# Optimization experiments

Measured on AMD Instinct MI355X. Metric: run time of the kernel, lower is better.

## Reference

```python
import jax, jax.numpy as jnp
import numpy as np

N_HEAD = 16

def setup_inputs() -> dict:
    key = jax.random.key(0)
    ks = jax.random.split(key, 5)
    C = 1024
    x = jax.random.normal(ks[0], (2, 2048, C), dtype=jnp.float32)
    w_attn = jax.random.normal(ks[1], (C, 3 * C), dtype=jnp.float32) * (C ** -0.5)
    b_attn = jax.random.normal(ks[2], (3 * C,), dtype=jnp.float32) * 0.02
    w_proj = jax.random.normal(ks[3], (C, C), dtype=jnp.float32) * (C ** -0.5)
    b_proj = jax.random.normal(ks[4], (C,), dtype=jnp.float32) * 0.02
    return {"x": x, "w_attn": w_attn, "b_attn": b_attn, "w_proj": w_proj, "b_proj": b_proj}

def reference(x, w_attn, b_attn, w_proj, b_proj):
    B, T, C = x.shape
    H = N_HEAD
    D = C // H  # head_dim
    qkv = x @ w_attn + b_attn  # [B,T,3C]
    q, k, v = jnp.split(qkv, 3, axis=-1)
    # [B,T,H,D] -> [B,H,T,D]
    q = q.reshape(B, T, H, D).transpose(0, 2, 1, 3)
    k = k.reshape(B, T, H, D).transpose(0, 2, 1, 3)
    v = v.reshape(B, T, H, D).transpose(0, 2, 1, 3)
    scale = 1.0 / np.sqrt(D).astype(np.float32)
    att = jnp.einsum('bhqd,bhkd->bhqk', q, k) * scale  # [B,H,T,T]
    causal = jnp.tril(jnp.ones((T, T), dtype=bool))
    att = jnp.where(causal, att, jnp.finfo(att.dtype).min)
    att = jax.nn.softmax(att, axis=-1)
    y = jnp.einsum('bhqk,bhkd->bhqd', att, v)  # [B,H,T,D]
    y = y.transpose(0, 2, 1, 3).reshape(B, T, C)
    return y @ w_proj + b_proj
```

## Files before the change

kernel.cpp:

```cpp
#include <hip/hip_runtime.h>
#include <hip/hip_bf16.h>
#include <stdint.h>

typedef __bf16 bf16x8 __attribute__((ext_vector_type(8)));
typedef __bf16 bf16x4 __attribute__((ext_vector_type(4)));
typedef float  f32x4  __attribute__((ext_vector_type(4)));

#define GLOBAL_AS __attribute__((address_space(1)))
#define LDS_AS    __attribute__((address_space(3)))

__device__ __forceinline__ void gld_lds16(const __bf16* g, __bf16* l) {
  __builtin_amdgcn_global_load_lds((GLOBAL_AS void*)g, (LDS_AS void*)l, 16, 0, 0);
}

#define QSCALE 0.18033688011116029f

__device__ __forceinline__ unsigned pk2(float a, float b) {
  unsigned short ua = __builtin_bit_cast(unsigned short, (__bf16)a);
  unsigned short ub = __builtin_bit_cast(unsigned short, (__bf16)b);
  return (unsigned)ua | ((unsigned)ub << 16);
}

union PackU { unsigned u[4]; bf16x8 v; };

__global__ __launch_bounds__(256) void cast_bf16_kernel(const float* __restrict__ src,
                                                        __bf16* __restrict__ dst, int n)
{
  int i = (blockIdx.x * 256 + threadIdx.x) * 8;
  if (i >= n) return;
  float4 a = *(const float4*)(src + i);
  float4 b = *(const float4*)(src + i + 4);
  bf16x8 o;
  o[0]=(__bf16)a.x; o[1]=(__bf16)a.y; o[2]=(__bf16)a.z; o[3]=(__bf16)a.w;
  o[4]=(__bf16)b.x; o[5]=(__bf16)b.y; o[6]=(__bf16)b.z; o[7]=(__bf16)b.w;
  *(bf16x8*)(dst + i) = o;
}

__global__ __launch_bounds__(256) void transpose_cast_kernel(const float* __restrict__ src,
                                                             __bf16* __restrict__ dst,
                                                             int R, int C)
{
  __shared__ float tile[32][33];
  int c0 = blockIdx.x * 32, r0 = blockIdx.y * 32;
  int tx = threadIdx.x & 31, ty = threadIdx.x >> 5;
  #pragma unroll
  for (int i = 0; i < 32; i += 8)
    tile[ty + i][tx] = src[(size_t)(r0 + ty + i) * C + (c0 + tx)];
  __syncthreads();
  #pragma unroll
  for (int i = 0; i < 32; i += 8)
    dst[(size_t)(c0 + ty + i) * R + (r0 + tx)] = (__bf16)tile[tx][ty + i];
}

template<int MODE, int BM>
__global__ __launch_bounds__(256, (BM == 128 ? 3 : 2))
void gemm_kernel(const __bf16* __restrict__ A,
                 const __bf16* __restrict__ Bt,
                 const float*  __restrict__ bias,
                 float* __restrict__ outF,
                 __bf16* __restrict__ qb,
                 __bf16* __restrict__ kb,
                 __bf16* __restrict__ vb,
                 int M, int N, int K)
{
  __shared__ __bf16 As[BM * 64];
  __shared__ __bf16 Bs[128 * 64];
  const int tid  = threadIdx.x;
  const int wave = tid >> 6, lane = tid & 63;
  const int lo = lane & 15, g4 = lane >> 4;
  const int bm = blockIdx.y * BM;
  const int bn = blockIdx.x * 128;
  const int wr = (wave >> 1) * (BM / 2);
  const int wc = (wave & 1) * 64;
  constexpr int MF = BM / 32;

  f32x4 acc[MF][4] = {};

  const int nkt = K >> 6;
  for (int kt = 0; kt < nkt; ++kt) {
    const int k0 = kt << 6;
    __syncthreads();
    #pragma unroll
    for (int j = 0; j < BM / 32; ++j) {
      int c = j * 256 + tid;
      int r = c >> 3, cc = c & 7;
      int cs = cc ^ (r & 7);
      gld_lds16(A + (size_t)(bm + r) * K + (k0 + cs * 8), As + c * 8);
    }
    #pragma unroll
    for (int j = 0; j < 4; ++j) {
      int c = j * 256 + tid;
      int r = c >> 3, cc = c & 7;
      int cs = cc ^ (r & 7);
      gld_lds16(Bt + (size_t)(bn + r) * K + (k0 + cs * 8), Bs + c * 8);
    }
    __syncthreads();
    #pragma unroll
    for (int ks = 0; ks < 2; ++ks) {
      bf16x8 af[MF], bfr[4];
      #pragma unroll
      for (int mf = 0; mf < MF; ++mf) {
        int row = wr + mf * 16 + lo;
        int ch = (ks * 4 + g4) ^ (row & 7);
        af[mf] = *(const bf16x8*)(As + row * 64 + ch * 8);
      }
      #pragma unroll
      for (int nf = 0; nf < 4; ++nf) {
        int row = wc + nf * 16 + lo;
        int ch = (ks * 4 + g4) ^ (row & 7);
        bfr[nf] = *(const bf16x8*)(Bs + row * 64 + ch * 8);
      }
      #pragma unroll
      for (int mf = 0; mf < MF; ++mf)
        #pragma unroll
        for (int nf = 0; nf < 4; ++nf)
          acc[mf][nf] = __builtin_amdgcn_mfma_f32_16x16x32_bf16(af[mf], bfr[nf], acc[mf][nf], 0, 0, 0);
    }
  }

  float bv[4];
  #pragma unroll
  for (int nf = 0; nf < 4; ++nf) bv[nf] = bias[bn + wc + nf * 16 + lo];

  if (MODE == 1) {
    #pragma unroll
    for (int mf = 0; mf < MF; ++mf)
      #pragma unroll
      for (int nf = 0; nf < 4; ++nf) {
        int col = bn + wc + nf * 16 + lo;
        #pragma unroll
        for (int j = 0; j < 4; ++j) {
          int row = bm + wr + mf * 16 + g4 * 4 + j;
          outF[(size_t)row * N + col] = acc[mf][nf][j] + bv[nf];
        }
      }
  } else {
    #pragma unroll
    for (int mf = 0; mf < MF; ++mf) {
      const int tbase = bm + wr + mf * 16 + g4 * 4;
      const int b = tbase >> 11, t = tbase & 2047;
      #pragma unroll
      for (int nf = 0; nf < 4; ++nf) {
        int n = bn + wc + nf * 16 + lo;
        int sel = n >> 10, hd = n & 1023;
        int h = hd >> 6, d = hd & 63;
        size_t bh = (size_t)(b * 16 + h);
        if (sel == 2) {
          bf16x4 pv;
          #pragma unroll
          for (int j = 0; j < 4; ++j) pv[j] = (__bf16)(acc[mf][nf][j] + bv[nf]);
          *(bf16x4*)(vb + (bh * 64 + d) * 2048 + t) = pv;
        } else if (sel == 0) {
          #pragma unroll
          for (int j = 0; j < 4; ++j)
            qb[(bh * 2048 + (size_t)(t + j)) * 64 + d] = (__bf16)((acc[mf][nf][j] + bv[nf]) * QSCALE);
        } else {
          #pragma unroll
          for (int j = 0; j < 4; ++j)
            kb[(bh * 2048 + (size_t)(t + j)) * 64 + d] = (__bf16)(acc[mf][nf][j] + bv[nf]);
        }
      }
    }
  }
}

__global__ __launch_bounds__(256, 4)
void attn_kernel(const __bf16* __restrict__ qg, const __bf16* __restrict__ kg,
                 const __bf16* __restrict__ vg, __bf16* __restrict__ yg)
{
  const int n = blockIdx.x;
  const int xcd = n & 7;
  const int w = n >> 3;
  const int quad = w >> 5;
  const int r = w & 31;
  const int bh = xcd + 8 * (r & 3);
  const int p = r >> 2;
  int strip;
  if      (quad == 0) strip = p;
  else if (quad == 1) strip = 31 - p;
  else if (quad == 2) strip = 8 + p;
  else                strip = 23 - p;
  const int b = bh >> 4, h = bh & 15;

  const int tid  = threadIdx.x;
  const int wave = tid >> 6;
  const int lane = tid & 63;
  const int l15  = lane & 15;
  const int g    = lane >> 4;
  const int sw   = l15 & 7;

  __shared__ __bf16 Kb[2][64 * 64];
  __shared__ __bf16 Vb[2][64 * 64];

  const __bf16* qbase = qg + (size_t)bh * 2048 * 64;
  const __bf16* kbase = kg + (size_t)bh * 2048 * 64;
  const __bf16* vbase = vg + (size_t)bh * 64 * 2048;

  const int q16 = strip * 64 + wave * 16 + l15;
  const bf16x8 qf0 = *(const bf16x8*)(qbase + (size_t)q16 * 64 + g * 8);
  const bf16x8 qf1 = *(const bf16x8*)(qbase + (size_t)q16 * 64 + 32 + g * 8);

  f32x4 o0 = {}, o1 = {}, o2 = {}, o3 = {}, osum = {};

  bf16x8 ones;
  #pragma unroll
  for (int j = 0; j < 8; ++j) ones[j] = (__bf16)1.0f;

  auto STAGE = [&](int kt, int bsel) {
    #pragma unroll
    for (int j = 0; j < 2; ++j) {
      int c = j * 256 + tid;
      int cr = c >> 3, cc = c & 7;
      int cs = cc ^ (cr & 7);
      int pr = (cr & 0x23) | ((cr & 0x10) >> 2) | ((cr & 0x0C) << 1);
      gld_lds16(kbase + (size_t)(kt * 64 + pr) * 64 + cs * 8, &Kb[bsel][0] + c * 8);
      gld_lds16(vbase + (size_t)cr * 2048 + (kt * 64 + cs * 8), &Vb[bsel][0] + c * 8);
    }
  };

  STAGE(0, 0);
  int cur = 0;

  for (int i = 0; i <= strip; ++i) {
    __syncthreads();
    if (i < strip) STAGE(i + 1, cur ^ 1);

    const __bf16* KL = &Kb[cur][0];
    f32x4 s0 = {}, s1 = {}, s2 = {}, s3 = {};
    {
      bf16x8 k00 = *(const bf16x8*)(KL + (0  + l15) * 64 + ((0 + g) ^ sw) * 8);
      bf16x8 k01 = *(const bf16x8*)(KL + (0  + l15) * 64 + ((4 + g) ^ sw) * 8);
      s0 = __builtin_amdgcn_mfma_f32_16x16x32_bf16(k00, qf0, s0, 0, 0, 0);
      s0 = __builtin_amdgcn_mfma_f32_16x16x32_bf16(k01, qf1, s0, 0, 0, 0);
      bf16x8 k10 = *(const bf16x8*)(KL + (16 + l15) * 64 + ((0 + g) ^ sw) * 8);
      bf16x8 k11 = *(const bf16x8*)(KL + (16 + l15) * 64 + ((4 + g) ^ sw) * 8);
      s1 = __builtin_amdgcn_mfma_f32_16x16x32_bf16(k10, qf0, s1, 0, 0, 0);
      s1 = __builtin_amdgcn_mfma_f32_16x16x32_bf16(k11, qf1, s1, 0, 0, 0);
      bf16x8 k20 = *(const bf16x8*)(KL + (32 + l15) * 64 + ((0 + g) ^ sw) * 8);
      bf16x8 k21 = *(const bf16x8*)(KL + (32 + l15) * 64 + ((4 + g) ^ sw) * 8);
      s2 = __builtin_amdgcn_mfma_f32_16x16x32_bf16(k20, qf0, s2, 0, 0, 0);
      s2 = __builtin_amdgcn_mfma_f32_16x16x32_bf16(k21, qf1, s2, 0, 0, 0);
      bf16x8 k30 = *(const bf16x8*)(KL + (48 + l15) * 64 + ((0 + g) ^ sw) * 8);
      bf16x8 k31 = *(const bf16x8*)(KL + (48 + l15) * 64 + ((4 + g) ^ sw) * 8);
      s3 = __builtin_amdgcn_mfma_f32_16x16x32_bf16(k30, qf0, s3, 0, 0, 0);
      s3 = __builtin_amdgcn_mfma_f32_16x16x32_bf16(k31, qf1, s3, 0, 0, 0);
    }

    if (i == strip) {
      const int qr = wave * 16 + l15;
      #pragma unroll
      for (int r2 = 0; r2 < 4; ++r2) {
        if (8 * g + r2          > qr) s0[r2] = -3.0e38f;
        if (8 * g + 4 + r2      > qr) s1[r2] = -3.0e38f;
        if (32 + 8 * g + r2     > qr) s2[r2] = -3.0e38f;
        if (32 + 8 * g + 4 + r2 > qr) s3[r2] = -3.0e38f;
      }
    }

    #pragma unroll
    for (int r2 = 0; r2 < 4; ++r2) s0[r2] = exp2f(s0[r2]);
    #pragma unroll
    for (int r2 = 0; r2 < 4; ++r2) s1[r2] = exp2f(s1[r2]);
    #pragma unroll
    for (int r2 = 0; r2 < 4; ++r2) s2[r2] = exp2f(s2[r2]);
    #pragma unroll
    for (int r2 = 0; r2 < 4; ++r2) s3[r2] = exp2f(s3[r2]);

    PackU pa0, pa1;
    pa0.u[0] = pk2(s0[0], s0[1]); pa0.u[1] = pk2(s0[2], s0[3]);
    pa0.u[2] = pk2(s1[0], s1[1]); pa0.u[3] = pk2(s1[2], s1[3]);
    pa1.u[0] = pk2(s2[0], s2[1]); pa1.u[1] = pk2(s2[2], s2[3]);
    pa1.u[2] = pk2(s3[0], s3[1]); pa1.u[3] = pk2(s3[2], s3[3]);

    osum = __builtin_amdgcn_mfma_f32_16x16x32_bf16(pa0.v, ones, osum, 0, 0, 0);
    osum = __builtin_amdgcn_mfma_f32_16x16x32_bf16(pa1.v, ones, osum, 0, 0, 0);

    const __bf16* VL = &Vb[cur][0];
    {
      bf16x8 v00 = *(const bf16x8*)(VL + (0  + l15) * 64 + ((0 + g) ^ sw) * 8);
      bf16x8 v01 = *(const bf16x8*)(VL + (0  + l15) * 64 + ((4 + g) ^ sw) * 8);
      o0 = __builtin_amdgcn_mfma_f32_16x16x32_bf16(pa0.v, v00, o0, 0, 0, 0);
      o0 = __builtin_amdgcn_mfma_f32_16x16x32_bf16(pa1.v, v01, o0, 0, 0, 0);
      bf16x8 v10 = *(const bf16x8*)(VL + (16 + l15) * 64 + ((0 + g) ^ sw) * 8);
      bf16x8 v11 = *(const bf16x8*)(VL + (16 + l15) * 64 + ((4 + g) ^ sw) * 8);
      o1 = __builtin_amdgcn_mfma_f32_16x16x32_bf16(pa0.v, v10, o1, 0, 0, 0);
      o1 = __builtin_amdgcn_mfma_f32_16x16x32_bf16(pa1.v, v11, o1, 0, 0, 0);
      bf16x8 v20 = *(const bf16x8*)(VL + (32 + l15) * 64 + ((0 + g) ^ sw) * 8);
      bf16x8 v21 = *(const bf16x8*)(VL + (32 + l15) * 64 + ((4 + g) ^ sw) * 8);
      o2 = __builtin_amdgcn_mfma_f32_16x16x32_bf16(pa0.v, v20, o2, 0, 0, 0);
      o2 = __builtin_amdgcn_mfma_f32_16x16x32_bf16(pa1.v, v21, o2, 0, 0, 0);
      bf16x8 v30 = *(const bf16x8*)(VL + (48 + l15) * 64 + ((0 + g) ^ sw) * 8);
      bf16x8 v31 = *(const bf16x8*)(VL + (48 + l15) * 64 + ((4 + g) ^ sw) * 8);
      o3 = __builtin_amdgcn_mfma_f32_16x16x32_bf16(pa0.v, v30, o3, 0, 0, 0);
      o3 = __builtin_amdgcn_mfma_f32_16x16x32_bf16(pa1.v, v31, o3, 0, 0, 0);
    }

    cur ^= 1;
  }

  #pragma unroll
  for (int r2 = 0; r2 < 4; ++r2) {
    float il = 1.0f / osum[r2];
    int trow = strip * 64 + wave * 16 + 4 * g + r2;
    __bf16* dst = yg + ((size_t)(b * 2048 + trow)) * 1024 + h * 64;
    dst[l15]      = (__bf16)(o0[r2] * il);
    dst[16 + l15] = (__bf16)(o1[r2] * il);
    dst[32 + l15] = (__bf16)(o2[r2] * il);
    dst[48 + l15] = (__bf16)(o3[r2] * il);
  }
}

extern "C" void kernel_launch(void* const* d_in, const int* in_sizes, int n_in,
                              void* d_out, int out_size, void* d_ws, size_t ws_size,
                              hipStream_t stream)
{
  const float* x      = (const float*)d_in[0];
  const float* w_attn = (const float*)d_in[1];
  const float* b_attn = (const float*)d_in[2];
  const float* w_proj = (const float*)d_in[3];
  const float* b_proj = (const float*)d_in[4];
  float* out = (float*)d_out;

  __bf16* xb  = (__bf16*)d_ws;
  __bf16* waT = xb  + (size_t)4096 * 1024;
  __bf16* wpT = waT + (size_t)3072 * 1024;
  __bf16* qb  = wpT + (size_t)1024 * 1024;
  __bf16* kb  = qb  + (size_t)32 * 2048 * 64;
  __bf16* vb  = kb  + (size_t)32 * 2048 * 64;
  __bf16* yb  = vb  + (size_t)32 * 2048 * 64;

  cast_bf16_kernel<<<2048, 256, 0, stream>>>(x, xb, 4096 * 1024);
  transpose_cast_kernel<<<dim3(96, 32), 256, 0, stream>>>(w_attn, waT, 1024, 3072);
  transpose_cast_kernel<<<dim3(32, 32), 256, 0, stream>>>(w_proj, wpT, 1024, 1024);
  gemm_kernel<0, 128><<<dim3(24, 32), 256, 0, stream>>>(xb, waT, b_attn, nullptr,
                                                        qb, kb, vb, 4096, 3072, 1024);
  attn_kernel<<<1024, 256, 0, stream>>>(qb, kb, vb, yb);
  gemm_kernel<1, 64><<<dim3(8, 64), 256, 0, stream>>>(yb, wpT, b_proj, out,
                                                      nullptr, nullptr, nullptr, 4096, 1024, 1024);
}
```

Measured before the change: 99.98 us.

## Balance causal attention with split-KV strips and remap QKV GEMM block order

The attention kernel now gives every block a fixed budget of roughly 16-17 key tiles. Blocks with t<16 finish a short strip, then process the first half of a long strip's keys. Blocks with t>=16 process the second half. Partial unnormalized outputs and row sums go to workspace and a new merge kernel combines them. The QKV GEMM also uses a 1D grid with a swizzled block-to-tile mapping to improve L2 locality across XCDs. This adds an extra kernel launch and partial-result traffic, and it reuses the x/weight workspace buffers for partials.

```diff
diff --git a/kernel.cpp b/kernel.cpp
--- a/kernel.cpp
+++ b/kernel.cpp
@@ -68,8 +68,15 @@
   const int tid  = threadIdx.x;
   const int wave = tid >> 6, lane = tid & 63;
   const int lo = lane & 15, g4 = lane >> 4;
-  const int bm = blockIdx.y * BM;
-  const int bn = blockIdx.x * 128;
+  int bm, bn;
+  if (MODE == 0) {
+    int bid = blockIdx.x;
+    int bm_i = (bid & 7) * 4 + ((bid >> 3) & 3);
+    int bn_i = bid >> 5;
+    bm = bm_i * 128; bn = bn_i * 128;
+  } else {
+    bm = blockIdx.y * BM; bn = blockIdx.x * 128;
+  }
   const int wr = (wave >> 1) * (BM / 2);
   const int wc = (wave & 1) * 64;
   constexpr int MF = BM / 32;
@@ -165,21 +172,15 @@
 }
 
 __global__ __launch_bounds__(256, 4)
-void attn_kernel(const __bf16* __restrict__ qg, const __bf16* __restrict__ kg,
-                 const __bf16* __restrict__ vg, __bf16* __restrict__ yg)
+void attn_kernel(const __bf16* __restrict__ qg_, const __bf16* __restrict__ kg,
+                 const __bf16* __restrict__ vg, __bf16* __restrict__ yg,
+                 __bf16* __restrict__ pY, float* __restrict__ pL)
 {
   const int n = blockIdx.x;
   const int xcd = n & 7;
-  const int w = n >> 3;
-  const int quad = w >> 5;
-  const int r = w & 31;
-  const int bh = xcd + 8 * (r & 3);
-  const int p = r >> 2;
-  int strip;
-  if      (quad == 0) strip = p;
-  else if (quad == 1) strip = 31 - p;
-  else if (quad == 2) strip = 8 + p;
-  else                strip = 23 - p;
+  const int m = n >> 3;
+  const int bh = xcd + 8 * (m & 3);
+  const int t = m >> 2;
   const int b = bh >> 4, h = bh & 15;
 
   const int tid  = threadIdx.x;
@@ -192,20 +193,25 @@
   __shared__ __bf16 Kb[2][64 * 64];
   __shared__ __bf16 Vb[2][64 * 64];
 
-  const __bf16* qbase = qg + (size_t)bh * 2048 * 64;
-  const __bf16* kbase = kg + (size_t)bh * 2048 * 64;
-  const __bf16* vbase = vg + (size_t)bh * 64 * 2048;
-
-  const int q16 = strip * 64 + wave * 16 + l15;
-  const bf16x8 qf0 = *(const bf16x8*)(qbase + (size_t)q16 * 64 + g * 8);
-  const bf16x8 qf1 = *(const bf16x8*)(qbase + (size_t)q16 * 64 + 32 + g * 8);
-
-  f32x4 o0 = {}, o1 = {}, o2 = {}, o3 = {}, osum = {};
+  const __bf16* qbase = qg_ + (size_t)bh * 2048 * 64;
+  const __bf16* kbase = kg  + (size_t)bh * 2048 * 64;
+  const __bf16* vbase = vg  + (size_t)bh * 64 * 2048;
+
+  bf16x8 qf0, qf1;
+  f32x4 o0, o1, o2, o3, osum;
 
   bf16x8 ones;
   #pragma unroll
   for (int j = 0; j < 8; ++j) ones[j] = (__bf16)1.0f;
 
+  auto LOADQ = [&](int strip) {
+    const int q16 = strip * 64 + wave * 16 + l15;
+    qf0 = *(const bf16x8*)(qbase + (size_t)q16 * 64 + g * 8);
+    qf1 = *(const bf16x8*)(qbase + (size_t)q16 * 64 + 32 + g * 8);
+  };
+  auto RESET = [&]() {
+    o0 = f32x4{}; o1 = f32x4{}; o2 = f32x4{}; o3 = f32x4{}; osum = f32x4{};
+  };
   auto STAGE = [&](int kt, int bsel) {
     #pragma unroll
     for (int j = 0; j < 2; ++j) {
@@ -218,13 +224,7 @@
     }
   };
 
-  STAGE(0, 0);
-  int cur = 0;
-
-  for (int i = 0; i <= strip; ++i) {
-    __syncthreads();
-    if (i < strip) STAGE(i + 1, cur ^ 1);
-
+  auto TILE = [&](int cur, bool diag) {
     const __bf16* KL = &Kb[cur][0];
     f32x4 s0 = {}, s1 = {}, s2 = {}, s3 = {};
     {
@@ -246,7 +246,7 @@
       s3 = __builtin_amdgcn_mfma_f32_16x16x32_bf16(k31, qf1, s3, 0, 0, 0);
     }
 
-    if (i == strip) {
+    if (diag) {
       const int qr = wave * 16 + l15;
       #pragma unroll
       for (int r2 = 0; r2 < 4; ++r2) {
@@ -294,20 +294,97 @@
       o3 = __builtin_amdgcn_mfma_f32_16x16x32_bf16(pa0.v, v30, o3, 0, 0, 0);
       o3 = __builtin_amdgcn_mfma_f32_16x16x32_bf16(pa1.v, v31, o3, 0, 0, 0);
     }
-
-    cur ^= 1;
+  };
+
+  auto WRITE_Y = [&](int strip) {
+    #pragma unroll
+    for (int r2 = 0; r2 < 4; ++r2) {
+      float il = 1.0f / osum[r2];
+      int trow = strip * 64 + wave * 16 + 4 * g + r2;
+      __bf16* dst = yg + ((size_t)(b * 2048 + trow)) * 1024 + h * 64;
+      dst[l15]      = (__bf16)(o0[r2] * il);
+      dst[16 + l15] = (__bf16)(o1[r2] * il);
+      dst[32 + l15] = (__bf16)(o2[r2] * il);
+      dst[48 + l15] = (__bf16)(o3[r2] * il);
+    }
+  };
+  auto WRITE_PART = [&](int slot) {
+    __bf16* po = pY + (size_t)slot * 4096;
+    #pragma unroll
+    for (int r2 = 0; r2 < 4; ++r2) {
+      int row = wave * 16 + 4 * g + r2;
+      __bf16* dst = po + row * 64;
+      dst[l15]      = (__bf16)o0[r2];
+      dst[16 + l15] = (__bf16)o1[r2];
+      dst[32 + l15] = (__bf16)o2[r2];
+      dst[48 + l15] = (__bf16)o3[r2];
+    }
+    if (l15 == 0) {
+      #pragma unroll
+      for (int r2 = 0; r2 < 4; ++r2)
+        pL[slot * 64 + wave * 16 + 4 * g + r2] = osum[r2];
+    }
+  };
+
+  int cur = 0;
+  if (t < 16) {
+    LOADQ(t); RESET();
+    STAGE(0, 0);
+    for (int j = 0; j < 17; ++j) {
+      __syncthreads();
+      if (j < 16) {
+        int nx = j + 1;
+        STAGE((nx <= t) ? nx : (nx + 15 - t), cur ^ 1);
+      }
+      if (j <= t) {
+        TILE(cur, j == t);
+        if (j == t) { WRITE_Y(t); LOADQ(31 - t); RESET(); }
+      } else {
+        TILE(cur, j == 16);
+      }
+      cur ^= 1;
+    }
+    WRITE_PART((bh * 16 + (15 - t)) * 2 + 1);
+  } else {
+    LOADQ(t); RESET();
+    STAGE(0, 0);
+    for (int j = 0; j < 16; ++j) {
+      __syncthreads();
+      if (j < 15) STAGE(j + 1, cur ^ 1);
+      TILE(cur, false);
+      cur ^= 1;
+    }
+    WRITE_PART((bh * 16 + (t - 16)) * 2);
   }
-
+}
+
+__global__ __launch_bounds__(256)
+void attn_merge_kernel(const __bf16* __restrict__ pY, const float* __restrict__ pL,
+                       __bf16* __restrict__ yg)
+{
+  const int us = blockIdx.x & 15, bh = blockIdx.x >> 4;
+  const int b = bh >> 4, h = bh & 15;
+  const int tid = threadIdx.x;
+  const int row = tid >> 2, d0 = (tid & 3) * 16;
+  const int slotA = (bh * 16 + us) * 2, slotB = slotA + 1;
+
+  float l = pL[slotA * 64 + row] + pL[slotB * 64 + row];
+  float inv = 1.0f / l;
+
+  const __bf16* pa = pY + (size_t)slotA * 4096 + row * 64 + d0;
+  const __bf16* pb = pY + (size_t)slotB * 4096 + row * 64 + d0;
+  __bf16* dst = yg + ((size_t)(b * 2048 + (16 + us) * 64 + row)) * 1024 + h * 64 + d0;
+
+  bf16x8 a0 = *(const bf16x8*)pa, a1 = *(const bf16x8*)(pa + 8);
+  bf16x8 b0 = *(const bf16x8*)pb, b1 = *(const bf16x8*)(pb + 8);
+  bf16x8 r0, r1;
   #pragma unroll
-  for (int r2 = 0; r2 < 4; ++r2) {
-    float il = 1.0f / osum[r2];
-    int trow = strip * 64 + wave * 16 + 4 * g + r2;
-    __bf16* dst = yg + ((size_t)(b * 2048 + trow)) * 1024 + h * 64;
-    dst[l15]      = (__bf16)(o0[r2] * il);
-    dst[16 + l15] = (__bf16)(o1[r2] * il);
-    dst[32 + l15] = (__bf16)(o2[r2] * il);
-    dst[48 + l15] = (__bf16)(o3[r2] * il);
+  for (int j = 0; j < 8; ++j) {
+    r0[j] = (__bf16)(((float)a0[j] + (float)b0[j]) * inv);
+    r1[j] = (__bf16)(((float)a1[j] + (float)b1[j]) * inv);
   }
+  *(bf16x8*)dst = r0;
+  *(bf16x8*)(dst + 8) = r1;
 }
 
 extern "C" void kernel_launch(void* const* d_in, const int* in_sizes, int n_in,
@@ -329,12 +406,16 @@
   __bf16* vb  = kb  + (size_t)32 * 2048 * 64;
   __bf16* yb  = vb  + (size_t)32 * 2048 * 64;
 
+  __bf16* pY = xb;
+  float*  pL = (float*)waT;
+
   cast_bf16_kernel<<<2048, 256, 0, stream>>>(x, xb, 4096 * 1024);
   transpose_cast_kernel<<<dim3(96, 32), 256, 0, stream>>>(w_attn, waT, 1024, 3072);
   transpose_cast_kernel<<<dim3(32, 32), 256, 0, stream>>>(w_proj, wpT, 1024, 1024);
-  gemm_kernel<0, 128><<<dim3(24, 32), 256, 0, stream>>>(xb, waT, b_attn, nullptr,
-                                                        qb, kb, vb, 4096, 3072, 1024);
-  attn_kernel<<<1024, 256, 0, stream>>>(qb, kb, vb, yb);
+  gemm_kernel<0, 128><<<768, 256, 0, stream>>>(xb, waT, b_attn, nullptr,
+                                               qb, kb, vb, 4096, 3072, 1024);
+  attn_kernel<<<1024, 256, 0, stream>>>(qb, kb, vb, yb, pY, pL);
+  attn_merge_kernel<<<512, 256, 0, stream>>>(pY, pL, yb);
   gemm_kernel<1, 64><<<dim3(8, 64), 256, 0, stream>>>(yb, wpT, b_proj, out,
                                                       nullptr, nullptr, nullptr, 4096, 1024, 1024);
 }
```

After: 99.80 us. Within noise of the previous version (-0.2%).

## Store K/V in MFMA fragment order and load directly from global in attention

Applied to the files above, without the earlier changes.

The QKV GEMM epilogue now writes K and V in a pre-swizzled per-64-row tile layout matching the MFMA operand fragments, so the attention kernel can read each lane's bf16x8 operands straight from global memory (L2) instead of staging through double-buffered LDS with barriers. The GEMM also gets a 1D grid with a remapped block index to group M tiles per XCD for better L2 locality. This removes LDS staging and __syncthreads per tile, but each wave now loads K/V independently from global, giving four times the global/L2 traffic per block and exposing load latency without an explicit prefetch pipeline.

```diff
diff --git a/kernel.cpp b/kernel.cpp
--- a/kernel.cpp
+++ b/kernel.cpp
@@ -59,8 +59,8 @@
                  const float*  __restrict__ bias,
                  float* __restrict__ outF,
                  __bf16* __restrict__ qb,
-                 __bf16* __restrict__ kb,
-                 __bf16* __restrict__ vb,
+                 __bf16* __restrict__ kfr,
+                 __bf16* __restrict__ vfr,
                  int M, int N, int K)
 {
   __shared__ __bf16 As[BM * 64];
@@ -68,8 +68,15 @@
   const int tid  = threadIdx.x;
   const int wave = tid >> 6, lane = tid & 63;
   const int lo = lane & 15, g4 = lane >> 4;
-  const int bm = blockIdx.y * BM;
-  const int bn = blockIdx.x * 128;
+  int bm, bn;
+  if (MODE == 0) {
+    int bid = blockIdx.x;
+    int bm_i = (bid & 7) * 4 + ((bid >> 3) & 3);
+    int bn_i = bid >> 5;
+    bm = bm_i * 128; bn = bn_i * 128;
+  } else {
+    bm = blockIdx.y * BM; bn = blockIdx.x * 128;
+  }
   const int wr = (wave >> 1) * (BM / 2);
   const int wc = (wave & 1) * 64;
   constexpr int MF = BM / 32;
@@ -139,6 +146,7 @@
     for (int mf = 0; mf < MF; ++mf) {
       const int tbase = bm + wr + mf * 16 + g4 * 4;
       const int b = tbase >> 11, t = tbase & 2047;
+      const int i_t = t >> 6;
       #pragma unroll
       for (int nf = 0; nf < 4; ++nf) {
         int n = bn + wc + nf * 16 + lo;
@@ -146,18 +154,27 @@
         int h = hd >> 6, d = hd & 63;
         size_t bh = (size_t)(b * 16 + h);
         if (sel == 2) {
+          int tt = t & 63;
+          int ks = tt >> 5, gv = (tt >> 3) & 3, j0 = tt & 7;
           bf16x4 pv;
           #pragma unroll
           for (int j = 0; j < 4; ++j) pv[j] = (__bf16)(acc[mf][nf][j] + bv[nf]);
-          *(bf16x4*)(vb + (bh * 64 + d) * 2048 + t) = pv;
+          *(bf16x4*)(vfr + bh * 131072 + i_t * 4096 + (d >> 4) * 1024 + ks * 512
+                     + (gv * 16 + (d & 15)) * 8 + j0) = pv;
         } else if (sel == 0) {
           #pragma unroll
           for (int j = 0; j < 4; ++j)
             qb[(bh * 2048 + (size_t)(t + j)) * 64 + d] = (__bf16)((acc[mf][nf][j] + bv[nf]) * QSCALE);
         } else {
+          int ksd = d >> 5, gk = (d >> 3) & 3, jd = d & 7;
           #pragma unroll
-          for (int j = 0; j < 4; ++j)
-            kb[(bh * 2048 + (size_t)(t + j)) * 64 + d] = (__bf16)(acc[mf][nf][j] + bv[nf]);
+          for (int j = 0; j < 4; ++j) {
+            int tt = (t + j) & 63;
+            int mb = 2 * (tt >> 5) + ((tt >> 2) & 1);
+            int m  = 8 * ((tt >> 4) & 1) + 4 * ((tt >> 3) & 1) + (tt & 3);
+            kfr[bh * 131072 + i_t * 4096 + mb * 1024 + ksd * 512 + (gk * 16 + m) * 8 + jd]
+                = (__bf16)(acc[mf][nf][j] + bv[nf]);
+          }
         }
       }
     }
@@ -165,8 +182,8 @@
 }
 
 __global__ __launch_bounds__(256, 4)
-void attn_kernel(const __bf16* __restrict__ qg, const __bf16* __restrict__ kg,
-                 const __bf16* __restrict__ vg, __bf16* __restrict__ yg)
+void attn_kernel(const __bf16* __restrict__ qg, const __bf16* __restrict__ kf_,
+                 const __bf16* __restrict__ vf_, __bf16* __restrict__ yg)
 {
   const int n = blockIdx.x;
   const int xcd = n & 7;
@@ -187,14 +204,10 @@
   const int lane = tid & 63;
   const int l15  = lane & 15;
   const int g    = lane >> 4;
-  const int sw   = l15 & 7;
-
-  __shared__ __bf16 Kb[2][64 * 64];
-  __shared__ __bf16 Vb[2][64 * 64];
 
   const __bf16* qbase = qg + (size_t)bh * 2048 * 64;
-  const __bf16* kbase = kg + (size_t)bh * 2048 * 64;
-  const __bf16* vbase = vg + (size_t)bh * 64 * 2048;
+  const __bf16* kb = kf_ + (size_t)bh * 131072 + lane * 8;
+  const __bf16* vb = vf_ + (size_t)bh * 131072 + lane * 8;
 
   const int q16 = strip * 64 + wave * 16 + l15;
   const bf16x8 qf0 = *(const bf16x8*)(qbase + (size_t)q16 * 64 + g * 8);
@@ -206,45 +219,37 @@
   #pragma unroll
   for (int j = 0; j < 8; ++j) ones[j] = (__bf16)1.0f;
 
-  auto STAGE = [&](int kt, int bsel) {
-    #pragma unroll
-    for (int j = 0; j < 2; ++j) {
-      int c = j * 256 + tid;
-      int cr = c >> 3, cc = c & 7;
-      int cs = cc ^ (cr & 7);
-      int pr = (cr & 0x23) | ((cr & 0x10) >> 2) | ((cr & 0x0C) << 1);
-      gld_lds16(kbase + (size_t)(kt * 64 + pr) * 64 + cs * 8, &Kb[bsel][0] + c * 8);
-      gld_lds16(vbase + (size_t)cr * 2048 + (kt * 64 + cs * 8), &Vb[bsel][0] + c * 8);
-    }
-  };
-
-  STAGE(0, 0);
-  int cur = 0;
-
   for (int i = 0; i <= strip; ++i) {
-    __syncthreads();
-    if (i < strip) STAGE(i + 1, cur ^ 1);
-
-    const __bf16* KL = &Kb[cur][0];
+    const __bf16* kt = kb + i * 4096;
+
+    bf16x8 k00 = *(const bf16x8*)(kt);
+    bf16x8 k01 = *(const bf16x8*)(kt + 512);
+    bf16x8 k10 = *(const bf16x8*)(kt + 1024);
+    bf16x8 k11 = *(const bf16x8*)(kt + 1536);
+    bf16x8 k20 = *(const bf16x8*)(kt + 2048);
+    bf16x8 k21 = *(const bf16x8*)(kt + 2560);
+    bf16x8 k30 = *(const bf16x8*)(kt + 3072);
+    bf16x8 k31 = *(const bf16x8*)(kt + 3584);
+
     f32x4 s0 = {}, s1 = {}, s2 = {}, s3 = {};
-    {
-      bf16x8 k00 = *(const bf16x8*)(KL + (0  + l15) * 64 + ((0 + g) ^ sw) * 8);
-      bf16x8 k01 = *(const bf16x8*)(KL + (0  + l15) * 64 + ((4 + g) ^ sw) * 8);
-      s0 = __builtin_amdgcn_mfma_f32_16x16x32_bf16(k00, qf0, s0, 0, 0, 0);
-      s0 = __builtin_amdgcn_mfma_f32_16x16x32_bf16(k01, qf1, s0, 0, 0, 0);
-      bf16x8 k10 = *(const bf16x8*)(KL + (16 + l15) * 64 + ((0 + g) ^ sw) * 8);
-      bf16x8 k11 = *(const bf16x8*)(KL + (16 + l15) * 64 + ((4 + g) ^ sw) * 8);
-      s1 = __builtin_amdgcn_mfma_f32_16x16x32_bf16(k10, qf0, s1, 0, 0, 0);
-      s1 = __builtin_amdgcn_mfma_f32_16x16x32_bf16(k11, qf1, s1, 0, 0, 0);
-      bf16x8 k20 = *(const bf16x8*)(KL + (32 + l15) * 64 + ((0 + g) ^ sw) * 8);
-      bf16x8 k21 = *(const bf16x8*)(KL + (32 + l15) * 64 + ((4 + g) ^ sw) * 8);
-      s2 = __builtin_amdgcn_mfma_f32_16x16x32_bf16(k20, qf0, s2, 0, 0, 0);
-      s2 = __builtin_amdgcn_mfma_f32_16x16x32_bf16(k21, qf1, s2, 0, 0, 0);
-      bf16x8 k30 = *(const bf16x8*)(KL + (48 + l15) * 64 + ((0 + g) ^ sw) * 8);
-      bf16x8 k31 = *(const bf16x8*)(KL + (48 + l15) * 64 + ((4 + g) ^ sw) * 8);
-      s3 = __builtin_amdgcn_mfma_f32_16x16x32_bf16(k30, qf0, s3, 0, 0, 0);
-      s3 = __builtin_amdgcn_mfma_f32_16x16x32_bf16(k31, qf1, s3, 0, 0, 0);
-    }
+    s0 = __builtin_amdgcn_mfma_f32_16x16x32_bf16(k00, qf0, s0, 0, 0, 0);
+    s0 = __builtin_amdgcn_mfma_f32_16x16x32_bf16(k01, qf1, s0, 0, 0, 0);
+    s1 = __builtin_amdgcn_mfma_f32_16x16x32_bf16(k10, qf0, s1, 0, 0, 0);
+    s1 = __builtin_amdgcn_mfma_f32_16x16x32_bf16(k11, qf1, s1, 0, 0, 0);
+    s2 = __builtin_amdgcn_mfma_f32_16x16x32_bf16(k20, qf0, s2, 0, 0, 0);
+    s2 = __builtin_amdgcn_mfma_f32_16x16x32_bf16(k21, qf1, s2, 0, 0, 0);
+    s3 = __builtin_amdgcn_mfma_f32_16x16x32_bf16(k30, qf0, s3, 0, 0, 0);
+    s3 = __builtin_amdgcn_mfma_f32_16x16x32_bf16(k31, qf1, s3, 0, 0, 0);
+
+    const __bf16* vt = vb + i * 4096;
+    bf16x8 v00 = *(const bf16x8*)(vt);
+    bf16x8 v01 = *(const bf16x8*)(vt + 512);
+    bf16x8 v10 = *(const bf16x8*)(vt + 1024);
+    bf16x8 v11 = *(const bf16x8*)(vt + 1536);
+    bf16x8 v20 = *(const bf16x8*)(vt + 2048);
+    bf16x8 v21 = *(const bf16x8*)(vt + 2560);
+    bf16x8 v30 = *(const bf16x8*)(vt + 3072);
+    bf16x8 v31 = *(const bf16x8*)(vt + 3584);
 
     if (i == strip) {
       const int qr = wave * 16 + l15;
@@ -275,27 +280,14 @@
     osum = __builtin_amdgcn_mfma_f32_16x16x32_bf16(pa0.v, ones, osum, 0, 0, 0);
     osum = __builtin_amdgcn_mfma_f32_16x16x32_bf16(pa1.v, ones, osum, 0, 0, 0);
 
-    const __bf16* VL = &Vb[cur][0];
-    {
-      bf16x8 v00 = *(const bf16x8*)(VL + (0  + l15) * 64 + ((0 + g) ^ sw) * 8);
-      bf16x8 v01 = *(const bf16x8*)(VL + (0  + l15) * 64 + ((4 + g) ^ sw) * 8);
-      o0 = __builtin_amdgcn_mfma_f32_16x16x32_bf16(pa0.v, v00, o0, 0, 0, 0);
-      o0 = __builtin_amdgcn_mfma_f32_16x16x32_bf16(pa1.v, v01, o0, 0, 0, 0);
-      bf16x8 v10 = *(const bf16x8*)(VL + (16 + l15) * 64 + ((0 + g) ^ sw) * 8);
-      bf16x8 v11 = *(const bf16x8*)(VL + (16 + l15) * 64 + ((4 + g) ^ sw) * 8);
-      o1 = __builtin_amdgcn_mfma_f32_16x16x32_bf16(pa0.v, v10, o1, 0, 0, 0);
-      o1 = __builtin_amdgcn_mfma_f32_16x16x32_bf16(pa1.v, v11, o1, 0, 0, 0);
-      bf16x8 v20 = *(const bf16x8*)(VL + (32 + l15) * 64 + ((0 + g) ^ sw) * 8);
-      bf16x8 v21 = *(const bf16x8*)(VL + (32 + l15) * 64 + ((4 + g) ^ sw) * 8);
-      o2 = __builtin_amdgcn_mfma_f32_16x16x32_bf16(pa0.v, v20, o2, 0, 0, 0);
-      o2 = __builtin_amdgcn_mfma_f32_16x16x32_bf16(pa1.v, v21, o2, 0, 0, 0);
-      bf16x8 v30 = *(const bf16x8*)(VL + (48 + l15) * 64 + ((0 + g) ^ sw) * 8);
-      bf16x8 v31 = *(const bf16x8*)(VL + (48 + l15) * 64 + ((4 + g) ^ sw) * 8);
-      o3 = __builtin_amdgcn_mfma_f32_16x16x32_bf16(pa0.v, v30, o3, 0, 0, 0);
-      o3 = __builtin_amdgcn_mfma_f32_16x16x32_bf16(pa1.v, v31, o3, 0, 0, 0);
-    }
-
-    cur ^= 1;
+    o0 = __builtin_amdgcn_mfma_f32_16x16x32_bf16(pa0.v, v00, o0, 0, 0, 0);
+    o0 = __builtin_amdgcn_mfma_f32_16x16x32_bf16(pa1.v, v01, o0, 0, 0, 0);
+    o1 = __builtin_amdgcn_mfma_f32_16x16x32_bf16(pa0.v, v10, o1, 0, 0, 0);
+    o1 = __builtin_amdgcn_mfma_f32_16x16x32_bf16(pa1.v, v11, o1, 0, 0, 0);
+    o2 = __builtin_amdgcn_mfma_f32_16x16x32_bf16(pa0.v, v20, o2, 0, 0, 0);
+    o2 = __builtin_amdgcn_mfma_f32_16x16x32_bf16(pa1.v, v21, o2, 0, 0, 0);
+    o3 = __builtin_amdgcn_mfma_f32_16x16x32_bf16(pa0.v, v30, o3, 0, 0, 0);
+    o3 = __builtin_amdgcn_mfma_f32_16x16x32_bf16(pa1.v, v31, o3, 0, 0, 0);
   }
 
   #pragma unroll
@@ -325,16 +317,16 @@
   __bf16* waT = xb  + (size_t)4096 * 1024;
   __bf16* wpT = waT + (size_t)3072 * 1024;
   __bf16* qb  = wpT + (size_t)1024 * 1024;
-  __bf16* kb  = qb  + (size_t)32 * 2048 * 64;
-  __bf16* vb  = kb  + (size_t)32 * 2048 * 64;
-  __bf16* yb  = vb  + (size_t)32 * 2048 * 64;
+  __bf16* kfr = qb  + (size_t)32 * 2048 * 64;
+  __bf16* vfr = kfr + (size_t)32 * 2048 * 64;
+  __bf16* yb  = vfr + (size_t)32 * 2048 * 64;
 
   cast_bf16_kernel<<<2048, 256, 0, stream>>>(x, xb, 4096 * 1024);
   transpose_cast_kernel<<<dim3(96, 32), 256, 0, stream>>>(w_attn, waT, 1024, 3072);
   transpose_cast_kernel<<<dim3(32, 32), 256, 0, stream>>>(w_proj, wpT, 1024, 1024);
-  gemm_kernel<0, 128><<<dim3(24, 32), 256, 0, stream>>>(xb, waT, b_attn, nullptr,
-                                                        qb, kb, vb, 4096, 3072, 1024);
-  attn_kernel<<<1024, 256, 0, stream>>>(qb, kb, vb, yb);
+  gemm_kernel<0, 128><<<768, 256, 0, stream>>>(xb, waT, b_attn, nullptr,
+                                               qb, kfr, vfr, 4096, 3072, 1024);
+  attn_kernel<<<1024, 256, 0, stream>>>(qb, kfr, vfr, yb);
   gemm_kernel<1, 64><<<dim3(8, 64), 256, 0, stream>>>(yb, wpT, b_proj, out,
                                                       nullptr, nullptr, nullptr, 4096, 1024, 1024);
 }
```

Measured after the change: 110.2 us. +10.2%, slower.
